# Kernel tuning notes

Hardware: AMD Instinct MI355X
Metric: run time of the kernel (lower is better)

The kernel has to match this reference:

```python
import jax, jax.numpy as jnp
import numpy as np

N_ENTITIES = 100000
N_EDGES = 500000
N_RELATIONS = 200
DIM = 64
HEADS = 4
POW_ITER = 5
ALPHA = 0.1
LEAKY_SLOPE = 0.01
EPS = 1e-16


def setup_inputs() -> dict:
    key = jax.random.key(0)
    ks = jax.random.split(key, 11)
    scale = 0.1
    return {
        "entity_embed": jax.random.normal(ks[0], (N_ENTITIES, DIM), jnp.float32),
        "relation_embed": jax.random.normal(ks[1], (N_RELATIONS, DIM), jnp.float32),
        "W_h": jax.random.normal(ks[2], (DIM, HEADS * DIM), jnp.float32) * scale,
        "W_t": jax.random.normal(ks[3], (DIM, HEADS * DIM), jnp.float32) * scale,
        "W_r": jax.random.normal(ks[4], (DIM, HEADS * DIM), jnp.float32) * scale,
        "att_h": jax.random.normal(ks[5], (HEADS, DIM), jnp.float32) * scale,
        "att_t": jax.random.normal(ks[6], (HEADS, DIM), jnp.float32) * scale,
        "att_r": jax.random.normal(ks[7], (HEADS, DIM), jnp.float32) * scale,
        "W_o": jax.random.normal(ks[8], (HEADS * DIM, DIM), jnp.float32) * scale,
        "edge_index": jax.random.randint(ks[9], (2, N_EDGES), 0, N_ENTITIES, jnp.int64),
        "edge_type": jax.random.randint(ks[10], (N_EDGES,), 0, N_RELATIONS, jnp.int64),
    }


def _segment_softmax(scores, seg_ids, num_segments):
    # scores: [E, heads]; softmax over edges sharing the same seg_id, per head
    m = jax.ops.segment_max(scores, seg_ids, num_segments=num_segments)
    e = jnp.exp(scores - m[seg_ids])
    denom = jax.ops.segment_sum(e, seg_ids, num_segments=num_segments)
    return e / (denom[seg_ids] + EPS)


def reference(entity_embed, relation_embed, W_h, W_t, W_r,
              att_h, att_t, att_r, W_o, edge_index, edge_type):
    head_ids, tail_ids = edge_index[0], edge_index[1]

    # per-edge gathered embeddings, projected per head: [E, heads, dim]
    Wh = (entity_embed[head_ids] @ W_h).reshape(-1, HEADS, DIM)
    Wt = (entity_embed[tail_ids] @ W_t).reshape(-1, HEADS, DIM)
    Wr = (relation_embed[edge_type] @ W_r).reshape(-1, HEADS, DIM)

    s_h = jnp.sum(jnp.tanh(Wh) * att_h[None], axis=-1)  # [E, heads]
    s_t = jnp.sum(jnp.tanh(Wt) * att_t[None], axis=-1)
    s_r = jnp.sum(jnp.tanh(Wr) * att_r[None], axis=-1)
    scores = jax.nn.leaky_relu(s_h + s_t + s_r, negative_slope=LEAKY_SLOPE)

    att = _segment_softmax(scores, head_ids, N_ENTITIES)  # [E, heads]
    A = (1.0 - ALPHA) * att

    # PPR power iteration, vectorized over heads: Z: [N, heads, dim]
    Z0 = entity_embed[:, None, :]  # [N, 1, dim]
    Z_init = jnp.broadcast_to(Z0, (N_ENTITIES, HEADS, DIM))

    def step(Z, _):
        msgs = A[:, :, None] * Z[tail_ids]  # [E, heads, dim]
        Z_new = jax.ops.segment_sum(msgs, head_ids, num_segments=N_ENTITIES) + ALPHA * Z0
        return Z_new, None

    Z, _ = jax.lax.scan(step, Z_init, None, length=POW_ITER)

    out = Z.reshape(N_ENTITIES, HEADS * DIM) @ W_o  # [N, dim]
    return out
```

## Files before the change

### kernel.cpp

```cpp
#include <hip/hip_runtime.h>
#include <hip/hip_fp16.h>
#include <math.h>

#define N_ENT 100000
#define N_EDGE 500000
#define N_REL 200

typedef short bf16x8 __attribute__((ext_vector_type(8)));
typedef _Float16 f16x8 __attribute__((ext_vector_type(8)));
typedef float f32x4 __attribute__((ext_vector_type(4)));

__device__ __forceinline__ float fast_tanh(float x) {
    float xc = fminf(x, 15.f);
    float e = __expf(2.f * xc);
    return (e - 1.f) / (e + 1.f);
}

__device__ __forceinline__ unsigned short f2bf(float f) {
    unsigned u = __float_as_uint(f);
    unsigned r = u + 0x7FFF + ((u >> 16) & 1);
    return (unsigned short)(r >> 16);
}

__device__ __forceinline__ uint2 pack_half4(const float4 v) {
    __half2 lo = __floats2half2_rn(v.x, v.y);
    __half2 hi = __floats2half2_rn(v.z, v.w);
    uint2 r;
    r.x = *reinterpret_cast<const unsigned int*>(&lo);
    r.y = *reinterpret_cast<const unsigned int*>(&hi);
    return r;
}

__device__ __forceinline__ float4 unpack_half4(uint2 u) {
    __half2 lo = *reinterpret_cast<const __half2*>(&u.x);
    __half2 hi = *reinterpret_cast<const __half2*>(&u.y);
    float2 a = __half22float2(lo);
    float2 b = __half22float2(hi);
    return make_float4(a.x, a.y, b.x, b.y);
}

__global__ __launch_bounds__(256) void cvt_emb_kernel(
    const float* __restrict__ in, unsigned short* __restrict__ out, int nquads)
{
    for (int i = blockIdx.x * 256 + threadIdx.x; i < nquads; i += gridDim.x * 256) {
        float4 v = ((const float4*)in)[i];
        ushort4 o;
        o.x = f2bf(v.x); o.y = f2bf(v.y); o.z = f2bf(v.z); o.w = f2bf(v.w);
        ((ushort4*)out)[i] = o;
    }
}

__global__ __launch_bounds__(256) void cvt_wT_kernel(
    const float* __restrict__ W0, const float* __restrict__ W1,
    unsigned short* __restrict__ wT)
{
    int idx = blockIdx.x * 256 + threadIdx.x;
    if (idx >= 2 * 256 * 64) return;
    int mat = idx >> 14;
    int rem = idx & 16383;
    int col = rem >> 6;
    int k   = rem & 63;
    const float* W = (mat == 0) ? W0 : W1;
    wT[idx] = f2bf(W[k * 256 + col]);
}

__global__ __launch_bounds__(256) void cvt_woT_kernel(
    const float* __restrict__ Wo, __half* __restrict__ woT)
{
    int idx = blockIdx.x * 256 + threadIdx.x;
    if (idx >= 64 * 256) return;
    int d = idx >> 8;
    int k = idx & 255;
    woT[idx] = __float2half(Wo[k * 64 + d]);
}

__global__ __launch_bounds__(256) void proj_mfma_kernel(
    const unsigned short* __restrict__ emb_bf,
    const unsigned short* __restrict__ wT,
    const float* __restrict__ att0, const float* __restrict__ att1,
    float* __restrict__ p0, float* __restrict__ p1, int nrows)
{
    const int wv   = threadIdx.x >> 6;
    const int lane = threadIdx.x & 63;
    const int r4   = lane >> 4;
    const int cl   = lane & 15;
    const int rowbase = blockIdx.x * 64 + wv * 16;

    int ra = min(rowbase + cl, nrows - 1);
    bf16x8 a0 = *(const bf16x8*)(emb_bf + (size_t)ra * 64 + 8 * r4);
    bf16x8 a1 = *(const bf16x8*)(emb_bf + (size_t)ra * 64 + 8 * r4 + 32);

#pragma unroll
    for (int mat = 0; mat < 2; ++mat) {
        const float* att = (mat == 0) ? att0 : att1;
        float* p         = (mat == 0) ? p0 : p1;
        float pacc[4][4];
#pragma unroll
        for (int head = 0; head < 4; ++head) {
            float vsum[4] = {0.f, 0.f, 0.f, 0.f};
#pragma unroll
            for (int sub = 0; sub < 4; ++sub) {
                int col = head * 64 + sub * 16 + cl;
                const unsigned short* wp =
                    wT + ((size_t)(mat * 256 + col)) * 64 + 8 * r4;
                bf16x8 b0 = *(const bf16x8*)(wp);
                bf16x8 b1 = *(const bf16x8*)(wp + 32);
                f32x4 c = {0.f, 0.f, 0.f, 0.f};
                c = __builtin_amdgcn_mfma_f32_16x16x32_bf16(a0, b0, c, 0, 0, 0);
                c = __builtin_amdgcn_mfma_f32_16x16x32_bf16(a1, b1, c, 0, 0, 0);
                float av = att[head * 64 + sub * 16 + cl];
#pragma unroll
                for (int j = 0; j < 4; ++j)
                    vsum[j] = fmaf(fast_tanh(c[j]), av, vsum[j]);
            }
#pragma unroll
            for (int j = 0; j < 4; ++j) {
                float v = vsum[j];
                v += __shfl_xor(v, 1, 64);
                v += __shfl_xor(v, 2, 64);
                v += __shfl_xor(v, 4, 64);
                v += __shfl_xor(v, 8, 64);
                pacc[head][j] = v;
            }
        }
        if (cl == 0) {
#pragma unroll
            for (int j = 0; j < 4; ++j) {
                int row = rowbase + r4 * 4 + j;
                if (row < nrows) {
                    *(float4*)(p + (size_t)row * 4) = make_float4(
                        pacc[0][j], pacc[1][j], pacc[2][j], pacc[3][j]);
                }
            }
        }
    }
}

__global__ __launch_bounds__(256) void proj_gemm_kernel(
    const float* __restrict__ emb,
    const float* __restrict__ W0,
    const float* __restrict__ att0,
    float* __restrict__ p0,
    int nrows)
{
    __shared__ float e_lds[64][68];
    __shared__ float w0_lds[64][64];
    __shared__ float red[4][4][64];

    const int t    = threadIdx.x;
    const int wv   = t >> 6;
    const int lane = t & 63;
    const int er   = t & 15;
    const int d0   = (t >> 4) * 4;
    const int base = blockIdx.x * 64;

#pragma unroll
    for (int i = 0; i < 4; ++i) {
        int f = t + 256 * i;
        int row = f >> 4, c4 = f & 15;
        int gr = min(base + row, nrows - 1);
        float4 v = *(const float4*)(emb + (size_t)gr * 64 + 4 * c4);
        *(float4*)&e_lds[row][4 * c4] = v;
    }

    float p0s[4][4];

    for (int head = 0; head < 4; ++head) {
        {
            int k0 = t >> 4, c4 = t & 15;
#pragma unroll
            for (int kk = 0; kk < 4; ++kk) {
                int k = k0 + 16 * kk;
                *(float4*)&w0_lds[k][4 * c4] =
                    *(const float4*)(W0 + (size_t)k * 256 + head * 64 + 4 * c4);
            }
        }
        __syncthreads();

        float acc0[4][4] = {};
        for (int k4 = 0; k4 < 16; ++k4) {
            float4 z0 = *(const float4*)&e_lds[er +  0][4 * k4];
            float4 z1 = *(const float4*)&e_lds[er + 16][4 * k4];
            float4 z2 = *(const float4*)&e_lds[er + 32][4 * k4];
            float4 z3 = *(const float4*)&e_lds[er + 48][4 * k4];
            const float zr[4][4] = {
                {z0.x, z0.y, z0.z, z0.w},
                {z1.x, z1.y, z1.z, z1.w},
                {z2.x, z2.y, z2.z, z2.w},
                {z3.x, z3.y, z3.z, z3.w}};
#pragma unroll
            for (int jj = 0; jj < 4; ++jj) {
                float4 w0v = *(const float4*)&w0_lds[4 * k4 + jj][d0];
#pragma unroll
                for (int i = 0; i < 4; ++i) {
                    float zj = zr[i][jj];
                    acc0[i][0] = fmaf(zj, w0v.x, acc0[i][0]);
                    acc0[i][1] = fmaf(zj, w0v.y, acc0[i][1]);
                    acc0[i][2] = fmaf(zj, w0v.z, acc0[i][2]);
                    acc0[i][3] = fmaf(zj, w0v.w, acc0[i][3]);
                }
            }
        }

        float4 av0 = *(const float4*)(att0 + head * 64 + d0);
#pragma unroll
        for (int i = 0; i < 4; ++i) {
            float v = fast_tanh(acc0[i][0]) * av0.x
                    + fast_tanh(acc0[i][1]) * av0.y
                    + fast_tanh(acc0[i][2]) * av0.z
                    + fast_tanh(acc0[i][3]) * av0.w;
            v += __shfl_xor(v, 16, 64);
            v += __shfl_xor(v, 32, 64);
            p0s[head][i] = v;
        }
        __syncthreads();
    }

    if (lane < 16) {
#pragma unroll
        for (int h = 0; h < 4; ++h)
#pragma unroll
            for (int i = 0; i < 4; ++i)
                red[wv][h][lane + 16 * i] = p0s[h][i];
    }
    __syncthreads();
    if (t < 64) {
        int row = base + t;
        if (row < nrows) {
            float4 pv;
            pv.x = red[0][0][t] + red[1][0][t] + red[2][0][t] + red[3][0][t];
            pv.y = red[0][1][t] + red[1][1][t] + red[2][1][t] + red[3][1][t];
            pv.z = red[0][2][t] + red[1][2][t] + red[2][2][t] + red[3][2][t];
            pv.w = red[0][3][t] + red[1][3][t] + red[2][3][t] + red[3][3][t];
            *(float4*)(p0 + (size_t)row * 4) = pv;
        }
    }
}

__global__ __launch_bounds__(256) void hist_kernel(
    const int* __restrict__ eidx, int* __restrict__ counts)
{
    int e = blockIdx.x * 256 + threadIdx.x;
    if (e >= N_EDGE) return;
    atomicAdd(&counts[eidx[e]], 1);
}

__global__ __launch_bounds__(1024) void scan_kernel(
    const int* __restrict__ counts, int* __restrict__ row_start)
{
    __shared__ int wsum[16];
    __shared__ int carry_s;
    const int lane = threadIdx.x & 63;
    const int wid  = threadIdx.x >> 6;
    if (threadIdx.x == 0) carry_s = 0;
    __syncthreads();
    for (int base = 0; base < N_ENT; base += 4096) {
        int i0 = base + (int)threadIdx.x * 4;
        int4 v = make_int4(0, 0, 0, 0);
        if (i0 + 3 < N_ENT) v = *(const int4*)(counts + i0);
        else {
            if (i0 + 0 < N_ENT) v.x = counts[i0 + 0];
            if (i0 + 1 < N_ENT) v.y = counts[i0 + 1];
            if (i0 + 2 < N_ENT) v.z = counts[i0 + 2];
            if (i0 + 3 < N_ENT) v.w = counts[i0 + 3];
        }
        int s1 = v.x + v.y, s2 = s1 + v.z, tsum = s2 + v.w;
        int incl = tsum;
#pragma unroll
        for (int off = 1; off < 64; off <<= 1) {
            int t = __shfl_up(incl, off, 64);
            if (lane >= off) incl += t;
        }
        if (lane == 63) wsum[wid] = incl;
        __syncthreads();
        int wave_off = 0;
#pragma unroll
        for (int w = 0; w < 16; ++w)
            wave_off += (w < wid) ? wsum[w] : 0;
        int carry = carry_s;
        int excl = carry + wave_off + (incl - tsum);
        if (i0 + 3 < N_ENT) {
            *(int4*)(row_start + i0) = make_int4(excl, excl + v.x, excl + s1, excl + s2);
        } else {
            if (i0 + 0 < N_ENT) row_start[i0 + 0] = excl;
            if (i0 + 1 < N_ENT) row_start[i0 + 1] = excl + v.x;
            if (i0 + 2 < N_ENT) row_start[i0 + 2] = excl + s1;
            if (i0 + 3 < N_ENT) row_start[i0 + 3] = excl + s2;
        }
        __syncthreads();
        if (threadIdx.x == 1023) carry_s = carry + wave_off + incl;
    }
    __syncthreads();
    if (threadIdx.x == 0) row_start[N_ENT] = carry_s;
}

__global__ __launch_bounds__(256) void scatter_score_kernel(
    const int* __restrict__ eidx, const int* __restrict__ etype,
    const float* __restrict__ ph, const float* __restrict__ pt,
    const float* __restrict__ pr,
    const int* __restrict__ row_start, int* __restrict__ cursor,
    int* __restrict__ csr_col, float* __restrict__ csr_a)
{
    int e = blockIdx.x * 256 + threadIdx.x;
    if (e >= N_EDGE) return;
    int hn = eidx[e];
    int tn = eidx[N_EDGE + e];
    int r  = etype[e];
    float4 a = *(const float4*)(ph + (size_t)hn * 4);
    float4 b = *(const float4*)(pt + (size_t)tn * 4);
    float4 c = *(const float4*)(pr + (size_t)r * 4);
    float s0 = a.x + b.x + c.x;
    float s1 = a.y + b.y + c.y;
    float s2 = a.z + b.z + c.z;
    float s3 = a.w + b.w + c.w;
    s0 = s0 >= 0.f ? s0 : 0.01f * s0;
    s1 = s1 >= 0.f ? s1 : 0.01f * s1;
    s2 = s2 >= 0.f ? s2 : 0.01f * s2;
    s3 = s3 >= 0.f ? s3 : 0.01f * s3;
    float4 ev = make_float4(__expf(s0), __expf(s1), __expf(s2), __expf(s3));
    int pos = row_start[hn] + atomicAdd(&cursor[hn], 1);
    csr_col[pos] = tn;
    *(float4*)(csr_a + (size_t)pos * 4) = ev;
}

__global__ __launch_bounds__(256) void normalize_kernel(
    const int* __restrict__ row_start, float* __restrict__ csr_a)
{
    const int wid  = threadIdx.x >> 6;
    const int lane = threadIdx.x & 63;
    const int n = blockIdx.x * 4 + wid;
    if (n >= N_ENT) return;
    const int s   = row_start[n];
    const int end = row_start[n + 1];
    const int nf  = (end - s) * 4;

    float sum = 0.f;
    for (int f = lane; f < nf; f += 64)
        sum += csr_a[(size_t)s * 4 + f];
#pragma unroll
    for (int off = 4; off < 64; off <<= 1)
        sum += __shfl_xor(sum, off, 64);
    float scale = 0.9f / (sum + 1e-16f);
    for (int f = lane; f < nf; f += 64)
        csr_a[(size_t)s * 4 + f] *= scale;
}

template <bool IN_HALF, bool OUT_HALF>
__global__ __launch_bounds__(256) void spmm_kernel(
    const void* __restrict__ Zin_v, const float* __restrict__ emb,
    const int* __restrict__ row_start, const int* __restrict__ csr_col,
    const float* __restrict__ csr_a, void* __restrict__ Zout_v)
{
    const int wave = threadIdx.x >> 6;
    const int lane = threadIdx.x & 63;
    const int n = blockIdx.x * 4 + wave;
    const int h = lane >> 4;
    const __half* Zin_h = (const __half*)Zin_v;

    const float4* e4 = (const float4*)emb;
    float4 zi = e4[(size_t)n * 16 + (lane & 15)];
    float4 acc0 = make_float4(0.1f * zi.x, 0.1f * zi.y, 0.1f * zi.z, 0.1f * zi.w);
    float4 acc1 = make_float4(0.f, 0.f, 0.f, 0.f);
    float4 acc2 = make_float4(0.f, 0.f, 0.f, 0.f);
    float4 acc3 = make_float4(0.f, 0.f, 0.f, 0.f);

    const int s   = row_start[n];
    const int end = row_start[n + 1];

    auto zrow = [&](int c) -> float4 {
        if (IN_HALF) {
            uint2 u = *(const uint2*)(Zin_h + (size_t)c * 256 + 4 * lane);
            return unpack_half4(u);
        } else {
            return *(const float4*)(emb + (size_t)c * 64 + 4 * (lane & 15));
        }
    };
    auto fma4 = [](float4& acc, float a, const float4& z) {
        acc.x = fmaf(a, z.x, acc.x);
        acc.y = fmaf(a, z.y, acc.y);
        acc.z = fmaf(a, z.z, acc.z);
        acc.w = fmaf(a, z.w, acc.w);
    };

    for (int b = s; b < end; b += 16) {
        const int nb = min(16, end - b);
        int   cl = (lane < nb) ? csr_col[b + lane] : 0;
        float al = (lane < nb * 4) ? csr_a[(size_t)b * 4 + lane] : 0.f;

        int j = 0;
        for (; j + 4 <= nb; j += 4) {
            int c0 = __shfl(cl, j + 0, 64);
            int c1 = __shfl(cl, j + 1, 64);
            int c2 = __shfl(cl, j + 2, 64);
            int c3 = __shfl(cl, j + 3, 64);
            float a0 = __shfl(al, (j + 0) * 4 + h, 64);
            float a1 = __shfl(al, (j + 1) * 4 + h, 64);
            float a2 = __shfl(al, (j + 2) * 4 + h, 64);
            float a3 = __shfl(al, (j + 3) * 4 + h, 64);
            float4 za = zrow(c0);
            float4 zb = zrow(c1);
            float4 zc = zrow(c2);
            float4 zd = zrow(c3);
            fma4(acc0, a0, za);
            fma4(acc1, a1, zb);
            fma4(acc2, a2, zc);
            fma4(acc3, a3, zd);
        }
        if (j + 0 < nb) {
            int c = __shfl(cl, j + 0, 64);
            float a = __shfl(al, (j + 0) * 4 + h, 64);
            float4 z = zrow(c);
            fma4(acc0, a, z);
        }
        if (j + 1 < nb) {
            int c = __shfl(cl, j + 1, 64);
            float a = __shfl(al, (j + 1) * 4 + h, 64);
            float4 z = zrow(c);
            fma4(acc1, a, z);
        }
        if (j + 2 < nb) {
            int c = __shfl(cl, j + 2, 64);
            float a = __shfl(al, (j + 2) * 4 + h, 64);
            float4 z = zrow(c);
            fma4(acc2, a, z);
        }
    }
    acc0.x += acc1.x + acc2.x + acc3.x;
    acc0.y += acc1.y + acc2.y + acc3.y;
    acc0.z += acc1.z + acc2.z + acc3.z;
    acc0.w += acc1.w + acc2.w + acc3.w;

    if (OUT_HALF)
        *(uint2*)((__half*)Zout_v + (size_t)n * 256 + 4 * lane) = pack_half4(acc0);
    else
        *(float4*)((float*)Zout_v + (size_t)n * 256 + 4 * lane) = acc0;
}

__global__ __launch_bounds__(256) void outproj_mfma_kernel(
    const __half* __restrict__ Z,
    const __half* __restrict__ woT,
    float* __restrict__ out)
{
    const int wv   = threadIdx.x >> 6;
    const int lane = threadIdx.x & 63;
    const int cl   = lane & 15;
    const int r4   = lane >> 4;
    const int rowbase = blockIdx.x * 64 + wv * 16;

    int ra = min(rowbase + cl, N_ENT - 1);
    const _Float16* zp = (const _Float16*)(Z + (size_t)ra * 256);
    f16x8 a[8];
#pragma unroll
    for (int ks = 0; ks < 8; ++ks)
        a[ks] = *(const f16x8*)(zp + ks * 32 + 8 * r4);

    const _Float16* wp = (const _Float16*)woT;
#pragma unroll
    for (int st = 0; st < 4; ++st) {
        f32x4 c = {0.f, 0.f, 0.f, 0.f};
        const _Float16* wcol = wp + (size_t)(st * 16 + cl) * 256 + 8 * r4;
#pragma unroll
        for (int ks = 0; ks < 8; ++ks) {
            f16x8 b = *(const f16x8*)(wcol + ks * 32);
            c = __builtin_amdgcn_mfma_f32_16x16x32_f16(a[ks], b, c, 0, 0, 0);
        }
#pragma unroll
        for (int j = 0; j < 4; ++j) {
            int row = rowbase + r4 * 4 + j;
            if (row < N_ENT)
                out[(size_t)row * 64 + st * 16 + cl] = c[j];
        }
    }
}

extern "C" void kernel_launch(void* const* d_in, const int* in_sizes, int n_in,
                              void* d_out, int out_size, void* d_ws, size_t ws_size,
                              hipStream_t stream)
{
    const float* entity = (const float*)d_in[0];
    const float* rel    = (const float*)d_in[1];
    const float* W_h    = (const float*)d_in[2];
    const float* W_t    = (const float*)d_in[3];
    const float* W_r    = (const float*)d_in[4];
    const float* att_h  = (const float*)d_in[5];
    const float* att_t  = (const float*)d_in[6];
    const float* att_r  = (const float*)d_in[7];
    const float* W_o    = (const float*)d_in[8];
    const int*   eidx   = (const int*)d_in[9];
    const int*   etype  = (const int*)d_in[10];
    float* out = (float*)d_out;

    char* ws = (char*)d_ws;
    size_t off = 0;
    auto alloc = [&](size_t bytes) -> void* {
        void* p = ws + off;
        off += (bytes + 255) & ~(size_t)255;
        return p;
    };
    float* p_h      = (float*)alloc((size_t)N_ENT * 4 * 4);
    float* p_t      = (float*)alloc((size_t)N_ENT * 4 * 4);
    float* p_r      = (float*)alloc((size_t)N_REL * 4 * 4);
    int*   counts   = (int*)alloc((size_t)N_ENT * 4);
    int*   row_start= (int*)alloc(((size_t)N_ENT + 1) * 4);
    int*   cursor   = (int*)alloc((size_t)N_ENT * 4);
    int*   csr_col  = (int*)alloc((size_t)N_EDGE * 4);
    float* csr_a    = (float*)alloc((size_t)N_EDGE * 4 * 4);
    __half* Zh_a    = (__half*)alloc((size_t)N_ENT * 256 * 2);
    __half* Zh_b    = (__half*)alloc((size_t)N_ENT * 256 * 2);
    unsigned short* emb_bf = (unsigned short*)alloc((size_t)N_ENT * 64 * 2);
    unsigned short* wT     = (unsigned short*)alloc((size_t)2 * 256 * 64 * 2);
    __half* woT     = (__half*)alloc((size_t)64 * 256 * 2);

    hipMemsetAsync(counts, 0, (size_t)N_ENT * 4, stream);
    hipMemsetAsync(cursor, 0, (size_t)N_ENT * 4, stream);

    cvt_emb_kernel<<<2048, 256, 0, stream>>>(entity, emb_bf, N_ENT * 64 / 4);
    cvt_wT_kernel<<<(2 * 256 * 64 + 255) / 256, 256, 0, stream>>>(W_h, W_t, wT);
    cvt_woT_kernel<<<(64 * 256 + 255) / 256, 256, 0, stream>>>(W_o, woT);

    proj_mfma_kernel<<<(N_ENT + 63) / 64, 256, 0, stream>>>(
        emb_bf, wT, att_h, att_t, p_h, p_t, N_ENT);
    proj_gemm_kernel<<<(N_REL + 63) / 64, 256, 0, stream>>>(
        rel, W_r, att_r, p_r, N_REL);

    hist_kernel<<<(N_EDGE + 255) / 256, 256, 0, stream>>>(eidx, counts);
    scan_kernel<<<1, 1024, 0, stream>>>(counts, row_start);
    scatter_score_kernel<<<(N_EDGE + 255) / 256, 256, 0, stream>>>(
        eidx, etype, p_h, p_t, p_r, row_start, cursor, csr_col, csr_a);
    normalize_kernel<<<(N_ENT + 3) / 4, 256, 0, stream>>>(row_start, csr_a);

    spmm_kernel<false, true ><<<N_ENT / 4, 256, 0, stream>>>(nullptr, entity, row_start, csr_col, csr_a, Zh_b);
    spmm_kernel<true,  true ><<<N_ENT / 4, 256, 0, stream>>>(Zh_b, entity, row_start, csr_col, csr_a, Zh_a);
    spmm_kernel<true,  true ><<<N_ENT / 4, 256, 0, stream>>>(Zh_a, entity, row_start, csr_col, csr_a, Zh_b);
    spmm_kernel<true,  true ><<<N_ENT / 4, 256, 0, stream>>>(Zh_b, entity, row_start, csr_col, csr_a, Zh_a);
    spmm_kernel<true,  true ><<<N_ENT / 4, 256, 0, stream>>>(Zh_a, entity, row_start, csr_col, csr_a, Zh_b);

    outproj_mfma_kernel<<<(N_ENT + 63) / 64, 256, 0, stream>>>(Zh_b, woT, out);
}
```

Before: 460.8 us.

## Fuse final SpMM iteration with output projection via shared-memory tile

The fifth power-iteration SpMM is merged with the W_o output projection. Each block computes 16 rows into LDS as fp16 and then runs MFMA against the transposed W_o, so the final Z never goes to global memory and one kernel launch is removed. Each wave now handles four rows one after another in the fused kernel, which lowers parallelism for that step. Separately, the tanh and normalize divisions are replaced with hardware reciprocal approximations.

```diff
diff --git a/kernel.cpp b/kernel.cpp
--- a/kernel.cpp
+++ b/kernel.cpp
@@ -13,7 +13,7 @@
 __device__ __forceinline__ float fast_tanh(float x) {
     float xc = fminf(x, 15.f);
     float e = __expf(2.f * xc);
-    return (e - 1.f) / (e + 1.f);
+    return 1.f - 2.f * __builtin_amdgcn_rcpf(e + 1.f);
 }
 
 __device__ __forceinline__ unsigned short f2bf(float f) {
@@ -340,23 +340,18 @@
 #pragma unroll
     for (int off = 4; off < 64; off <<= 1)
         sum += __shfl_xor(sum, off, 64);
-    float scale = 0.9f / (sum + 1e-16f);
+    float scale = 0.9f * __builtin_amdgcn_rcpf(sum + 1e-16f);
     for (int f = lane; f < nf; f += 64)
         csr_a[(size_t)s * 4 + f] *= scale;
 }
 
-template <bool IN_HALF, bool OUT_HALF>
-__global__ __launch_bounds__(256) void spmm_kernel(
-    const void* __restrict__ Zin_v, const float* __restrict__ emb,
+template <bool IN_HALF>
+__device__ __forceinline__ float4 spmm_row(
+    int n, int lane, int h,
+    const __half* __restrict__ Zin_h, const float* __restrict__ emb,
     const int* __restrict__ row_start, const int* __restrict__ csr_col,
-    const float* __restrict__ csr_a, void* __restrict__ Zout_v)
-{
-    const int wave = threadIdx.x >> 6;
-    const int lane = threadIdx.x & 63;
-    const int n = blockIdx.x * 4 + wave;
-    const int h = lane >> 4;
-    const __half* Zin_h = (const __half*)Zin_v;
-
+    const float* __restrict__ csr_a)
+{
     const float4* e4 = (const float4*)emb;
     float4 zi = e4[(size_t)n * 16 + (lane & 15)];
     float4 acc0 = make_float4(0.1f * zi.x, 0.1f * zi.y, 0.1f * zi.z, 0.1f * zi.w);
@@ -409,67 +404,81 @@
         if (j + 0 < nb) {
             int c = __shfl(cl, j + 0, 64);
             float a = __shfl(al, (j + 0) * 4 + h, 64);
-            float4 z = zrow(c);
-            fma4(acc0, a, z);
+            fma4(acc0, a, zrow(c));
         }
         if (j + 1 < nb) {
             int c = __shfl(cl, j + 1, 64);
             float a = __shfl(al, (j + 1) * 4 + h, 64);
-            float4 z = zrow(c);
-            fma4(acc1, a, z);
+            fma4(acc1, a, zrow(c));
         }
         if (j + 2 < nb) {
             int c = __shfl(cl, j + 2, 64);
             float a = __shfl(al, (j + 2) * 4 + h, 64);
-            float4 z = zrow(c);
-            fma4(acc2, a, z);
+            fma4(acc2, a, zrow(c));
         }
     }
     acc0.x += acc1.x + acc2.x + acc3.x;
     acc0.y += acc1.y + acc2.y + acc3.y;
     acc0.z += acc1.z + acc2.z + acc3.z;
     acc0.w += acc1.w + acc2.w + acc3.w;
-
-    if (OUT_HALF)
-        *(uint2*)((__half*)Zout_v + (size_t)n * 256 + 4 * lane) = pack_half4(acc0);
-    else
-        *(float4*)((float*)Zout_v + (size_t)n * 256 + 4 * lane) = acc0;
-}
-
-__global__ __launch_bounds__(256) void outproj_mfma_kernel(
-    const __half* __restrict__ Z,
+    return acc0;
+}
+
+template <bool IN_HALF>
+__global__ __launch_bounds__(256) void spmm_kernel(
+    const void* __restrict__ Zin_v, const float* __restrict__ emb,
+    const int* __restrict__ row_start, const int* __restrict__ csr_col,
+    const float* __restrict__ csr_a, void* __restrict__ Zout_v)
+{
+    const int wave = threadIdx.x >> 6;
+    const int lane = threadIdx.x & 63;
+    const int n = blockIdx.x * 4 + wave;
+    const int h = lane >> 4;
+    float4 acc = spmm_row<IN_HALF>(n, lane, h, (const __half*)Zin_v, emb,
+                                   row_start, csr_col, csr_a);
+    *(uint2*)((__half*)Zout_v + (size_t)n * 256 + 4 * lane) = pack_half4(acc);
+}
+
+__global__ __launch_bounds__(256) void spmm_out_fused_kernel(
+    const __half* __restrict__ Zin, const float* __restrict__ emb,
+    const int* __restrict__ row_start, const int* __restrict__ csr_col,
+    const float* __restrict__ csr_a,
     const __half* __restrict__ woT,
     float* __restrict__ out)
 {
+    __shared__ _Float16 zl[16][264];
     const int wv   = threadIdx.x >> 6;
     const int lane = threadIdx.x & 63;
-    const int cl   = lane & 15;
-    const int r4   = lane >> 4;
-    const int rowbase = blockIdx.x * 64 + wv * 16;
-
-    int ra = min(rowbase + cl, N_ENT - 1);
-    const _Float16* zp = (const _Float16*)(Z + (size_t)ra * 256);
+    const int h    = lane >> 4;
+    const int base = blockIdx.x * 16;
+
+#pragma unroll
+    for (int rr = 0; rr < 4; ++rr) {
+        int n = base + wv * 4 + rr;
+        float4 acc = spmm_row<true>(n, lane, h, Zin, emb,
+                                    row_start, csr_col, csr_a);
+        *(uint2*)&zl[wv * 4 + rr][4 * lane] = pack_half4(acc);
+    }
+    __syncthreads();
+
+    const int cl = lane & 15;
+    const int r4 = lane >> 4;
     f16x8 a[8];
 #pragma unroll
     for (int ks = 0; ks < 8; ++ks)
-        a[ks] = *(const f16x8*)(zp + ks * 32 + 8 * r4);
-
-    const _Float16* wp = (const _Float16*)woT;
-#pragma unroll
-    for (int st = 0; st < 4; ++st) {
-        f32x4 c = {0.f, 0.f, 0.f, 0.f};
-        const _Float16* wcol = wp + (size_t)(st * 16 + cl) * 256 + 8 * r4;
-#pragma unroll
-        for (int ks = 0; ks < 8; ++ks) {
-            f16x8 b = *(const f16x8*)(wcol + ks * 32);
-            c = __builtin_amdgcn_mfma_f32_16x16x32_f16(a[ks], b, c, 0, 0, 0);
-        }
-#pragma unroll
-        for (int j = 0; j < 4; ++j) {
-            int row = rowbase + r4 * 4 + j;
-            if (row < N_ENT)
-                out[(size_t)row * 64 + st * 16 + cl] = c[j];
-        }
+        a[ks] = *(const f16x8*)&zl[cl][ks * 32 + 8 * r4];
+
+    const _Float16* wcol = (const _Float16*)woT + (size_t)(wv * 16 + cl) * 256 + 8 * r4;
+    f32x4 c = {0.f, 0.f, 0.f, 0.f};
+#pragma unroll
+    for (int ks = 0; ks < 8; ++ks) {
+        f16x8 b = *(const f16x8*)(wcol + ks * 32);
+        c = __builtin_amdgcn_mfma_f32_16x16x32_f16(a[ks], b, c, 0, 0, 0);
+    }
+#pragma unroll
+    for (int j = 0; j < 4; ++j) {
+        int row = base + r4 * 4 + j;
+        out[(size_t)row * 64 + wv * 16 + cl] = c[j];
     }
 }
 
@@ -529,11 +538,10 @@
         eidx, etype, p_h, p_t, p_r, row_start, cursor, csr_col, csr_a);
     normalize_kernel<<<(N_ENT + 3) / 4, 256, 0, stream>>>(row_start, csr_a);
 
-    spmm_kernel<false, true ><<<N_ENT / 4, 256, 0, stream>>>(nullptr, entity, row_start, csr_col, csr_a, Zh_b);
-    spmm_kernel<true,  true ><<<N_ENT / 4, 256, 0, stream>>>(Zh_b, entity, row_start, csr_col, csr_a, Zh_a);
-    spmm_kernel<true,  true ><<<N_ENT / 4, 256, 0, stream>>>(Zh_a, entity, row_start, csr_col, csr_a, Zh_b);
-    spmm_kernel<true,  true ><<<N_ENT / 4, 256, 0, stream>>>(Zh_b, entity, row_start, csr_col, csr_a, Zh_a);
-    spmm_kernel<true,  true ><<<N_ENT / 4, 256, 0, stream>>>(Zh_a, entity, row_start, csr_col, csr_a, Zh_b);
-
-    outproj_mfma_kernel<<<(N_ENT + 63) / 64, 256, 0, stream>>>(Zh_b, woT, out);
-}
+    spmm_kernel<false><<<N_ENT / 4, 256, 0, stream>>>(nullptr, entity, row_start, csr_col, csr_a, Zh_b);
+    spmm_kernel<true ><<<N_ENT / 4, 256, 0, stream>>>(Zh_b, entity, row_start, csr_col, csr_a, Zh_a);
+    spmm_kernel<true ><<<N_ENT / 4, 256, 0, stream>>>(Zh_a, entity, row_start, csr_col, csr_a, Zh_b);
+    spmm_kernel<true ><<<N_ENT / 4, 256, 0, stream>>>(Zh_b, entity, row_start, csr_col, csr_a, Zh_a);
+    spmm_out_fused_kernel<<<N_ENT / 16, 256, 0, stream>>>(
+        Zh_a, entity, row_start, csr_col, csr_a, woT, out);
+}
```

After: 439.4 us. 1.05x faster.
